# Kernel optimization log

Measured on AMD Instinct MI355X. Metric: run time of the kernel, lower is better.

The kernel has to match this reference:

```python
import jax, jax.numpy as jnp
import numpy as np

B, S, D, H = 4, 2048, 1024, 16
DK = D // H


def setup_inputs() -> dict:
    key = jax.random.key(0)
    ks = jax.random.split(key, 5)
    scale = 1.0 / np.sqrt(D)
    return {
        "x": jax.random.normal(ks[0], (B, S, D), dtype=jnp.float32),
        "w_q": jax.random.normal(ks[1], (D, D), dtype=jnp.float32) * scale,
        "w_k": jax.random.normal(ks[2], (D, D), dtype=jnp.float32) * scale,
        "w_v": jax.random.normal(ks[3], (D, D), dtype=jnp.float32) * scale,
        "w_o": jax.random.normal(ks[4], (D, D), dtype=jnp.float32) * scale,
        "b_o": jnp.zeros((D,), dtype=jnp.float32),
    }


def reference(x, w_q, w_k, w_v, w_o, b_o):
    b, s, d = x.shape
    # Projections (torch Linear: x @ W.T); split into heads -> [b, h, s, dk]
    q = (x @ w_q.T).reshape(b, s, H, DK).transpose(0, 2, 1, 3)
    k = (x @ w_k.T).reshape(b, s, H, DK).transpose(0, 2, 1, 3)
    v = (x @ w_v.T).reshape(b, s, H, DK).transpose(0, 2, 1, 3)
    # Scores [b, h, s, s]; causal mask (strict upper triangle -> -inf), then scale.
    scores = jnp.einsum("bhqd,bhkd->bhqk", q, k)
    causal = jnp.triu(jnp.ones((s, s), dtype=bool), k=1)
    scores = jnp.where(causal, -jnp.inf, scores)
    attn = jax.nn.softmax(scores / np.sqrt(DK), axis=-1)
    out = jnp.einsum("bhqk,bhkd->bhqd", attn, v)
    out = out.transpose(0, 2, 1, 3).reshape(b, s, d)
    return out @ w_o.T + b_o
```

## Files before the change

kernel.cpp:

```cpp
#include <hip/hip_runtime.h>
#include <hip/hip_bf16.h>
#include <math.h>

#define GLOBAL_AS __attribute__((address_space(1)))
#define LDS_AS __attribute__((address_space(3)))

typedef __bf16 bf16x8 __attribute__((ext_vector_type(8)));
typedef __bf16 bf16x4 __attribute__((ext_vector_type(4)));
typedef float f32x4 __attribute__((ext_vector_type(4)));
typedef float f32x16 __attribute__((ext_vector_type(16)));
typedef unsigned short u16x8 __attribute__((ext_vector_type(8)));

static constexpr int BB = 4, SS = 2048, DD = 1024, HH = 16, DKK = 64;
static constexpr int MM = BB * SS;
static constexpr int NQKV = 3 * DD;
static constexpr int NQT = SS / 128;

__device__ inline unsigned int cvt_pk_bf16(float lo, float hi) {
  unsigned int r;
  asm("v_cvt_pk_bf16_f32 %0, %1, %2" : "=v"(r) : "v"(lo), "v"(hi));
  return r;
}

__global__ __launch_bounds__(256) void cvt_kernel(const float* __restrict__ in,
                                                  __bf16* __restrict__ out,
                                                  int n4) {
  int i = blockIdx.x * blockDim.x + threadIdx.x;
  if (i < n4) {
    float4 v = reinterpret_cast<const float4*>(in)[i];
    bf16x4 o;
    o[0] = (__bf16)v.x; o[1] = (__bf16)v.y; o[2] = (__bf16)v.z; o[3] = (__bf16)v.w;
    *reinterpret_cast<bf16x4*>(out + (size_t)i * 4) = o;
  }
}

__global__ __launch_bounds__(256) void cvtw_kernel(const float* __restrict__ w_q,
                                                   const float* __restrict__ w_k,
                                                   const float* __restrict__ w_v,
                                                   const float* __restrict__ w_o,
                                                   __bf16* __restrict__ w_qkv,
                                                   __bf16* __restrict__ w_obf) {
  const int sel = blockIdx.y;
  const float* src = (sel == 0) ? w_q : (sel == 1) ? w_k : (sel == 2) ? w_v : w_o;
  __bf16* dst = (sel < 3) ? (w_qkv + (size_t)sel * DD * DD) : w_obf;
  int i = blockIdx.x * blockDim.x + threadIdx.x;
  float4 v = reinterpret_cast<const float4*>(src)[i];
  bf16x4 o;
  o[0] = (__bf16)v.x; o[1] = (__bf16)v.y; o[2] = (__bf16)v.z; o[3] = (__bf16)v.w;
  *reinterpret_cast<bf16x4*>(dst + (size_t)i * 4) = o;
}

template <int MODE>
__global__ __launch_bounds__(512, 1) void gemm8p(const unsigned short* __restrict__ A,
                                                 const unsigned short* __restrict__ Bm,
                                                 void* __restrict__ Cout,
                                                 const float* __restrict__ bias,
                                                 unsigned short* __restrict__ vt,
                                                 int Ndim, int K) {
  __shared__ __align__(16) unsigned short Asm[2 * 2 * 4096];
  __shared__ __align__(16) unsigned short Bsm[2 * 2 * 8192];
  const int tid = threadIdx.x, wid = tid >> 6, ln = tid & 63;
  const int wm = wid >> 2, wn = wid & 3;
  const int cl = ln & 15, ck = ln >> 4;

  const int gx = gridDim.x;
  const int nwg = gx * gridDim.y;
  const int qch = nwg >> 3;
  int lid = blockIdx.y * gx + blockIdx.x;
  lid = (lid & 7) * qch + (lid >> 3);
  const int bn0 = (lid % gx) * 256;
  const int bm0 = (lid / gx) * 128;

  const int KT = K >> 6;
  const int sr = tid >> 2;
  const int scol = ((tid & 3) ^ (sr & 3)) << 3;
  const int sc8 = (ck ^ (cl & 3)) << 3;

  f32x4 acc[4][4] = {};

  auto stage_group = [&](int buf, int kt, int kk) {
    const int k0 = kt * 64 + kk * 32;
    const unsigned short* ga = A + (size_t)(bm0 + sr) * K + k0 + scol;
    __builtin_amdgcn_global_load_lds((GLOBAL_AS void*)ga,
        (LDS_AS void*)(Asm + (buf * 2 + kk) * 4096 + wid * 512), 16, 0, 0);
#pragma unroll
    for (int j = 0; j < 2; ++j) {
      const unsigned short* gb = Bm + (size_t)(bn0 + j * 128 + sr) * K + k0 + scol;
      __builtin_amdgcn_global_load_lds((GLOBAL_AS void*)gb,
          (LDS_AS void*)(Bsm + (buf * 2 + kk) * 8192 + j * 4096 + wid * 512), 16, 0, 0);
    }
  };

  auto phase = [&](int p, int kk, int g_buf, int g_kt, int g_kk, bool g_issue, int vm) {
    bf16x8 af[4], bfr[4];
    const unsigned short* ab = Asm + (p * 2 + kk) * 4096;
    const unsigned short* bb = Bsm + (p * 2 + kk) * 8192;
#pragma unroll
    for (int mf = 0; mf < 4; ++mf)
      af[mf] = *reinterpret_cast<const bf16x8*>(ab + (wm * 64 + mf * 16 + cl) * 32 + sc8);
#pragma unroll
    for (int nf = 0; nf < 4; ++nf)
      bfr[nf] = *reinterpret_cast<const bf16x8*>(bb + (wn * 64 + nf * 16 + cl) * 32 + sc8);
    if (g_issue) stage_group(g_buf, g_kt, g_kk);
    __builtin_amdgcn_s_barrier();
    __builtin_amdgcn_s_setprio(1);
#pragma unroll
    for (int mf = 0; mf < 4; ++mf)
#pragma unroll
      for (int nf = 0; nf < 4; ++nf)
        acc[mf][nf] = __builtin_amdgcn_mfma_f32_16x16x32_bf16(af[mf], bfr[nf], acc[mf][nf], 0, 0, 0);
    __builtin_amdgcn_s_setprio(0);
    if (vm == 6)      asm volatile("s_waitcnt vmcnt(6)" ::: "memory");
    else if (vm == 3) asm volatile("s_waitcnt vmcnt(3)" ::: "memory");
    else if (vm == 0) asm volatile("s_waitcnt vmcnt(0)" ::: "memory");
    __builtin_amdgcn_s_barrier();
  };

  stage_group(0, 0, 0);
  stage_group(0, 0, 1);
  stage_group(1, 1, 0);
  asm volatile("s_waitcnt vmcnt(6)" ::: "memory");
  __builtin_amdgcn_s_barrier();

  for (int kt = 0; kt < KT; ++kt) {
    const int p = kt & 1;
    const bool i0 = (kt + 1 < KT);
    const bool i1 = (kt + 2 < KT);
    phase(p, 0, p ^ 1, kt + 1, 1, i0, i0 ? 6 : 0);
    phase(p, 1, p, kt + 2, 0, i1, (kt < KT - 1) ? (i1 ? 6 : 3) : -1);
  }

#pragma unroll
  for (int mf = 0; mf < 4; ++mf) {
#pragma unroll
    for (int nf = 0; nf < 4; ++nf) {
      const int col = bn0 + wn * 64 + nf * 16 + cl;
      if constexpr (MODE == 2) {
        if (col >= 2 * DD) {
          const int hcol = col - 2 * DD;
          const int hh = hcol >> 6, dk = hcol & 63;
          const int row0 = bm0 + wm * 64 + mf * 16 + ck * 4;
          const int bb_ = row0 >> 11, s0 = row0 & 2047;
          bf16x4 pv;
#pragma unroll
          for (int r = 0; r < 4; ++r) pv[r] = (__bf16)acc[mf][nf][r];
          *reinterpret_cast<bf16x4*>(vt + ((size_t)((bb_ * HH + hh) * 64 + dk)) * SS + s0) = pv;
          continue;
        }
      }
#pragma unroll
      for (int r = 0; r < 4; ++r) {
        const int row = bm0 + wm * 64 + mf * 16 + ck * 4 + r;
        float v = acc[mf][nf][r];
        if constexpr (MODE == 0) {
          ((float*)Cout)[(size_t)row * Ndim + col] = v + bias[col];
        } else {
          if (col < DD) v *= 0.18033688011112042f;
          ((__bf16*)Cout)[(size_t)row * Ndim + col] = (__bf16)v;
        }
      }
    }
  }
}

__global__ __launch_bounds__(256) void attn_kernel(const unsigned short* __restrict__ qkv,
                                                   const unsigned short* __restrict__ vt,
                                                   unsigned short* __restrict__ attn_out) {
  const int pi = blockIdx.x, h = blockIdx.y, b = blockIdx.z;
  const int tid = threadIdx.x, wv = tid >> 6, ln = tid & 63;
  const int l31 = ln & 31, hi = ln >> 5;
  const int bh = b * HH + h;

  __shared__ __align__(16) unsigned short Ks[2][64 * 64];
  __shared__ __align__(16) unsigned short Vs[2][64 * 64];

  bf16x8 vones;
#pragma unroll
  for (int j = 0; j < 8; ++j) vones[j] = (__bf16)1.0f;

  auto stage = [&](int bsel, int kv0s) {
#pragma unroll
    for (int i = 0; i < 2; ++i) {
      int idx = wv * 2 + i;
      int row = idx * 8 + (ln >> 3);
      int sch = (ln & 7) ^ (row & 7);
      const unsigned short* gk = qkv + ((size_t)(b * SS + kv0s + row) * NQKV + DD + h * DKK + sch * 8);
      __builtin_amdgcn_global_load_lds((GLOBAL_AS void*)gk, (LDS_AS void*)(&Ks[bsel][idx * 512]), 16, 0, 0);
      const unsigned short* gv = vt + ((size_t)(bh * 64 + row) * SS + kv0s + sch * 8);
      __builtin_amdgcn_global_load_lds((GLOBAL_AS void*)gv, (LDS_AS void*)(&Vs[bsel][idx * 512]), 16, 0, 0);
    }
  };

  auto process = [&](int qt) {
    const int q0w = qt * 128 + wv * 32;
    const int qq = q0w + l31;

    bf16x8 qf[4];
#pragma unroll
    for (int kkk = 0; kkk < 4; ++kkk)
      qf[kkk] = *reinterpret_cast<const bf16x8*>(
          qkv + (size_t)(b * SS + qq) * NQKV + h * DKK + kkk * 16 + hi * 8);

    f32x16 ot[2] = {};
    f32x16 lsum = {};
    float mrow = -INFINITY;

    const int nt = 2 * qt + 2;
    stage(0, 0);
    __syncthreads();
    int buf = 0;

    for (int t = 0; t < nt; ++t) {
      const int kv0 = t * 64;
      if (t + 1 < nt) stage(buf ^ 1, (t + 1) * 64);

      if (kv0 <= q0w + 31) {
        const unsigned short* kb = &Ks[buf][0];
        const unsigned short* vb = &Vs[buf][0];

        f32x16 st[2];
        __builtin_amdgcn_s_setprio(1);
#pragma unroll
        for (int cc = 0; cc < 2; ++cc) {
          f32x16 z = {};
#pragma unroll
          for (int kkk = 0; kkk < 4; ++kkk) {
            bf16x8 kf = *reinterpret_cast<const bf16x8*>(
                kb + (cc * 32 + l31) * 64 + (((kkk * 2 + hi) ^ (l31 & 7)) * 8));
            z = __builtin_amdgcn_mfma_f32_32x32x16_bf16(kf, qf[kkk], z, 0, 0, 0);
          }
          st[cc] = z;
        }
        __builtin_amdgcn_s_setprio(0);

        if (kv0 + 63 > q0w) {
          const int kvb = kv0 + 4 * hi;
#pragma unroll
          for (int cc = 0; cc < 2; ++cc)
#pragma unroll
            for (int r = 0; r < 16; ++r) {
              const int kv = kvb + cc * 32 + (r & 3) + 8 * (r >> 2);
              st[cc][r] = (kv <= qq) ? st[cc][r] : -INFINITY;
            }
        }

        float tm = st[0][0];
#pragma unroll
        for (int r = 1; r < 16; ++r) tm = fmaxf(tm, st[0][r]);
#pragma unroll
        for (int r = 0; r < 16; ++r) tm = fmaxf(tm, st[1][r]);
        tm = fmaxf(tm, __shfl_xor(tm, 32));

        if (__any(tm - mrow > 8.0f)) {
          float mn = fmaxf(mrow, tm);
          float al = __builtin_amdgcn_exp2f(mrow - mn);
          mrow = mn;
          lsum *= al;
          ot[0] *= al;
          ot[1] *= al;
        }

#pragma unroll
        for (int cc = 0; cc < 2; ++cc)
#pragma unroll
          for (int r = 0; r < 16; ++r)
            st[cc][r] = __builtin_amdgcn_exp2f(st[cc][r] - mrow);

        unsigned int pk[2][4], pk2[2][4];
#pragma unroll
        for (int cc = 0; cc < 2; ++cc)
#pragma unroll
          for (int g = 0; g < 4; ++g) {
            pk[cc][g]  = cvt_pk_bf16(st[cc][4 * g + 0], st[cc][4 * g + 1]);
            pk2[cc][g] = cvt_pk_bf16(st[cc][4 * g + 2], st[cc][4 * g + 3]);
          }

        __builtin_amdgcn_s_setprio(1);
#pragma unroll
        for (int ks = 0; ks < 4; ++ks) {
          const int cc = ks >> 1, g0 = 2 * (ks & 1), g1 = g0 + 1;
          unsigned int Aw = pk[cc][g0], Bw = pk[cc][g1];
          asm volatile("v_permlane32_swap_b32 %0, %1" : "+v"(Aw), "+v"(Bw));
          unsigned int A2 = pk2[cc][g0], B2 = pk2[cc][g1];
          asm volatile("v_permlane32_swap_b32 %0, %1" : "+v"(A2), "+v"(B2));
          union { unsigned int u[4]; bf16x8 v; } pb;
          pb.u[0] = Aw; pb.u[1] = A2; pb.u[2] = Bw; pb.u[3] = B2;
          lsum = __builtin_amdgcn_mfma_f32_32x32x16_bf16(vones, pb.v, lsum, 0, 0, 0);
#pragma unroll
          for (int dc = 0; dc < 2; ++dc) {
            bf16x8 vf = *reinterpret_cast<const bf16x8*>(
                vb + (dc * 32 + l31) * 64 + (((ks * 2 + hi) ^ (l31 & 7)) * 8));
            ot[dc] = __builtin_amdgcn_mfma_f32_32x32x16_bf16(vf, pb.v, ot[dc], 0, 0, 0);
          }
        }
        __builtin_amdgcn_s_setprio(0);
      }

      __syncthreads();
      buf ^= 1;
    }

    const float inv = 1.0f / lsum[0];
    __bf16* aout = (__bf16*)attn_out + (size_t)(b * SS + qq) * DD + h * DKK;
#pragma unroll
    for (int dc = 0; dc < 2; ++dc)
#pragma unroll
      for (int g = 0; g < 4; ++g) {
        uint2 pw;
        pw.x = cvt_pk_bf16(ot[dc][4 * g + 0] * inv, ot[dc][4 * g + 1] * inv);
        pw.y = cvt_pk_bf16(ot[dc][4 * g + 2] * inv, ot[dc][4 * g + 3] * inv);
        *reinterpret_cast<uint2*>(aout + dc * 32 + 4 * hi + 8 * g) = pw;
      }
  };

  process(NQT - 1 - pi);
  process(pi);
}

extern "C" void kernel_launch(void* const* d_in, const int* in_sizes, int n_in,
                              void* d_out, int out_size, void* d_ws, size_t ws_size,
                              hipStream_t stream) {
  const float* x = (const float*)d_in[0];
  const float* w_q = (const float*)d_in[1];
  const float* w_k = (const float*)d_in[2];
  const float* w_v = (const float*)d_in[3];
  const float* w_o = (const float*)d_in[4];
  const float* b_o = (const float*)d_in[5];
  float* out = (float*)d_out;

  unsigned short* ws = (unsigned short*)d_ws;
  unsigned short* x_bf = ws;
  unsigned short* w_qkv = x_bf + (size_t)MM * DD;
  unsigned short* w_obf = w_qkv + (size_t)NQKV * DD;
  unsigned short* qkv = w_obf + (size_t)DD * DD;
  unsigned short* vt = qkv + (size_t)MM * NQKV;
  unsigned short* attn = vt + (size_t)BB * HH * DKK * SS;

  cvt_kernel<<<(MM * DD / 4 + 255) / 256, 256, 0, stream>>>(x, (__bf16*)x_bf, MM * DD / 4);
  cvtw_kernel<<<dim3(DD * DD / 4 / 256, 4), 256, 0, stream>>>(w_q, w_k, w_v, w_o,
                                                              (__bf16*)w_qkv, (__bf16*)w_obf);

  gemm8p<2><<<dim3(NQKV / 256, MM / 128), 512, 0, stream>>>(x_bf, w_qkv, qkv, nullptr, vt, NQKV, DD);

  attn_kernel<<<dim3(NQT / 2, HH, BB), 256, 0, stream>>>(qkv, vt, attn);

  gemm8p<0><<<dim3(DD / 256, MM / 128), 512, 0, stream>>>(attn, w_obf, out, b_o, nullptr, DD, DD);
}
```

Measured before the change: 188.9 us.

## Use 256x256 tiled GEMM with interleaved LDS pipeline for QKV projection

Replaces the 128x256-tile QKV projection GEMM with a dedicated 256x256-tile kernel. It uses an 8-phase schedule that interleaves global-to-LDS loads of the next K-step with MFMA work on the current one, and raises wave priority around the MFMA blocks. The larger tile doubles operand reuse per byte loaded and halves the workgroup count to 384. The cost is more registers and LDS per block, fewer workgroups for the 256 CUs (tail imbalance), and many barriers. The output GEMM is de-templated and keeps the old kernel.

```diff
diff --git a/kernel.cpp b/kernel.cpp
--- a/kernel.cpp
+++ b/kernel.cpp
@@ -50,12 +50,161 @@
   *reinterpret_cast<bf16x4*>(dst + (size_t)i * 4) = o;
 }
 
-template <int MODE>
+__global__ __launch_bounds__(512, 1) void gemm256(const unsigned short* __restrict__ A,
+                                                  const unsigned short* __restrict__ Bm,
+                                                  unsigned short* __restrict__ qkv,
+                                                  unsigned short* __restrict__ vt,
+                                                  int Ndim, int K) {
+  __shared__ __align__(16) unsigned short SA[2][2][8192];
+  __shared__ __align__(16) unsigned short SB[2][2][8192];
+  const int tid = threadIdx.x, wid = tid >> 6, ln = tid & 63;
+  const int wm = wid >> 2, wn = wid & 3;
+  const int cl = ln & 15, ck = ln >> 4;
+
+  const int gx = gridDim.x, nwg = gx * gridDim.y;
+  const int qch = nwg >> 3;
+  int lid = blockIdx.y * gx + blockIdx.x;
+  lid = (lid & 7) * qch + (lid >> 3);
+  const int bn0 = (lid % gx) * 256;
+  const int bm0 = (lid / gx) * 256;
+
+  const int KT = K >> 6;
+  const int srow = tid >> 3;
+  const int scol8 = (((tid & 7) ^ (srow & 7)) << 3);
+  int chk[2];
+  chk[0] = ((ck ^ (cl & 7)) << 3);
+  chk[1] = (((4 + ck) ^ (cl & 7)) << 3);
+
+  f32x4 acc[8][4] = {};
+  bf16x8 aR[4][2], bRa[2][2], bRb[2][2];
+
+  auto stA = [&](int t, int qa) {
+    const unsigned short* g = A + (size_t)(bm0 + qa * 64 + srow) * K + t * 64 + scol8;
+    __builtin_amdgcn_global_load_lds((GLOBAL_AS void*)g,
+        (LDS_AS void*)(&SA[t & 1][qa >> 1][(qa & 1) * 4096 + tid * 8]), 16, 0, 0);
+  };
+  auto stB = [&](int t, int qb) {
+    const unsigned short* g = Bm + (size_t)(bn0 + qb * 64 + srow) * K + t * 64 + scol8;
+    __builtin_amdgcn_global_load_lds((GLOBAL_AS void*)g,
+        (LDS_AS void*)(&SB[t & 1][qb >> 1][(qb & 1) * 4096 + tid * 8]), 16, 0, 0);
+  };
+  auto ldA = [&](int buf, int rh) {
+    const unsigned short* base = &SA[buf][wm][0];
+#pragma unroll
+    for (int rf = 0; rf < 4; ++rf) {
+      const int row = rh * 64 + rf * 16 + cl;
+#pragma unroll
+      for (int kk = 0; kk < 2; ++kk)
+        aR[rf][kk] = *reinterpret_cast<const bf16x8*>(base + row * 64 + chk[kk]);
+    }
+  };
+  auto ldB = [&](int buf, int chalf, bf16x8 (&br)[2][2]) {
+    const unsigned short* base = &SB[buf][wn >> 1][0];
+#pragma unroll
+    for (int cf = 0; cf < 2; ++cf) {
+      const int row = (wn & 1) * 64 + chalf * 32 + cf * 16 + cl;
+#pragma unroll
+      for (int kk = 0; kk < 2; ++kk)
+        br[cf][kk] = *reinterpret_cast<const bf16x8*>(base + row * 64 + chk[kk]);
+    }
+  };
+  auto MF = [&](int rh, int chalf, bf16x8 (&br)[2][2]) {
+    __builtin_amdgcn_s_setprio(1);
+#pragma unroll
+    for (int rf = 0; rf < 4; ++rf)
+#pragma unroll
+      for (int cf = 0; cf < 2; ++cf)
+#pragma unroll
+        for (int kk = 0; kk < 2; ++kk)
+          acc[rh * 4 + rf][chalf * 2 + cf] = __builtin_amdgcn_mfma_f32_16x16x32_bf16(
+              aR[rf][kk], br[cf][kk], acc[rh * 4 + rf][chalf * 2 + cf], 0, 0, 0);
+    __builtin_amdgcn_s_setprio(0);
+  };
+
+  stB(0, 0); stB(0, 1); stB(0, 2); stB(0, 3);
+  stA(0, 0); stA(0, 2); stA(0, 1); stA(0, 3);
+  asm volatile("s_waitcnt vmcnt(2)" ::: "memory");
+  __builtin_amdgcn_s_barrier();
+
+  const int HKT = KT >> 1;
+  for (int it = 0; it < HKT; ++it) {
+    const int t1 = 2 * it + 1, v = 2 * it + 2;
+    const bool hv = (v < KT);
+    ldA(0, 0); ldB(0, 0, bRa);
+    stB(t1, 0); stB(t1, 1);
+    __builtin_amdgcn_s_barrier();
+    MF(0, 0, bRa);
+    __builtin_amdgcn_s_barrier();
+    ldB(0, 1, bRb);
+    stB(t1, 2); stB(t1, 3);
+    __builtin_amdgcn_s_barrier();
+    MF(0, 1, bRb);
+    asm volatile("s_waitcnt vmcnt(4)" ::: "memory");
+    __builtin_amdgcn_s_barrier();
+    ldA(0, 1);
+    stA(t1, 0); stA(t1, 2);
+    __builtin_amdgcn_s_barrier();
+    MF(1, 1, bRb);
+    __builtin_amdgcn_s_barrier();
+    stA(t1, 1); stA(t1, 3);
+    __builtin_amdgcn_s_barrier();
+    MF(1, 0, bRa);
+    asm volatile("s_waitcnt vmcnt(2)" ::: "memory");
+    __builtin_amdgcn_s_barrier();
+    ldA(1, 0); ldB(1, 0, bRa);
+    if (hv) { stB(v, 0); stB(v, 1); }
+    __builtin_amdgcn_s_barrier();
+    MF(0, 0, bRa);
+    __builtin_amdgcn_s_barrier();
+    ldB(1, 1, bRb);
+    if (hv) { stB(v, 2); stB(v, 3); }
+    __builtin_amdgcn_s_barrier();
+    MF(0, 1, bRb);
+    if (hv) asm volatile("s_waitcnt vmcnt(4)" ::: "memory");
+    else    asm volatile("s_waitcnt vmcnt(0)" ::: "memory");
+    __builtin_amdgcn_s_barrier();
+    ldA(1, 1);
+    if (hv) { stA(v, 0); stA(v, 2); }
+    __builtin_amdgcn_s_barrier();
+    MF(1, 1, bRb);
+    __builtin_amdgcn_s_barrier();
+    if (hv) { stA(v, 1); stA(v, 3); }
+    __builtin_amdgcn_s_barrier();
+    MF(1, 0, bRa);
+    if (hv) asm volatile("s_waitcnt vmcnt(2)" ::: "memory");
+    __builtin_amdgcn_s_barrier();
+  }
+
+#pragma unroll
+  for (int rf8 = 0; rf8 < 8; ++rf8) {
+#pragma unroll
+    for (int cf4 = 0; cf4 < 4; ++cf4) {
+      const int col = bn0 + wn * 64 + cf4 * 16 + cl;
+      const int row0 = bm0 + wm * 128 + rf8 * 16 + ck * 4;
+      if (col >= 2 * DD) {
+        const int hcol = col - 2 * DD;
+        const int hh = hcol >> 6, dk = hcol & 63;
+        const int bb_ = row0 >> 11, s0 = row0 & 2047;
+        bf16x4 pv;
+#pragma unroll
+        for (int r = 0; r < 4; ++r) pv[r] = (__bf16)acc[rf8][cf4][r];
+        *reinterpret_cast<bf16x4*>(vt + ((size_t)((bb_ * HH + hh) * 64 + dk)) * SS + s0) = pv;
+      } else {
+#pragma unroll
+        for (int r = 0; r < 4; ++r) {
+          float vv = acc[rf8][cf4][r];
+          if (col < DD) vv *= 0.18033688011112042f;
+          ((__bf16*)qkv)[(size_t)(row0 + r) * Ndim + col] = (__bf16)vv;
+        }
+      }
+    }
+  }
+}
+
 __global__ __launch_bounds__(512, 1) void gemm8p(const unsigned short* __restrict__ A,
                                                  const unsigned short* __restrict__ Bm,
-                                                 void* __restrict__ Cout,
+                                                 float* __restrict__ Cout,
                                                  const float* __restrict__ bias,
-                                                 unsigned short* __restrict__ vt,
                                                  int Ndim, int K) {
   __shared__ __align__(16) unsigned short Asm[2 * 2 * 4096];
   __shared__ __align__(16) unsigned short Bsm[2 * 2 * 8192];
@@ -135,29 +284,10 @@
 #pragma unroll
     for (int nf = 0; nf < 4; ++nf) {
       const int col = bn0 + wn * 64 + nf * 16 + cl;
-      if constexpr (MODE == 2) {
-        if (col >= 2 * DD) {
-          const int hcol = col - 2 * DD;
-          const int hh = hcol >> 6, dk = hcol & 63;
-          const int row0 = bm0 + wm * 64 + mf * 16 + ck * 4;
-          const int bb_ = row0 >> 11, s0 = row0 & 2047;
-          bf16x4 pv;
-#pragma unroll
-          for (int r = 0; r < 4; ++r) pv[r] = (__bf16)acc[mf][nf][r];
-          *reinterpret_cast<bf16x4*>(vt + ((size_t)((bb_ * HH + hh) * 64 + dk)) * SS + s0) = pv;
-          continue;
-        }
-      }
 #pragma unroll
       for (int r = 0; r < 4; ++r) {
         const int row = bm0 + wm * 64 + mf * 16 + ck * 4 + r;
-        float v = acc[mf][nf][r];
-        if constexpr (MODE == 0) {
-          ((float*)Cout)[(size_t)row * Ndim + col] = v + bias[col];
-        } else {
-          if (col < DD) v *= 0.18033688011112042f;
-          ((__bf16*)Cout)[(size_t)row * Ndim + col] = (__bf16)v;
-        }
+        Cout[(size_t)row * Ndim + col] = acc[mf][nf][r] + bias[col];
       }
     }
   }
@@ -340,9 +470,9 @@
   cvtw_kernel<<<dim3(DD * DD / 4 / 256, 4), 256, 0, stream>>>(w_q, w_k, w_v, w_o,
                                                               (__bf16*)w_qkv, (__bf16*)w_obf);
 
-  gemm8p<2><<<dim3(NQKV / 256, MM / 128), 512, 0, stream>>>(x_bf, w_qkv, qkv, nullptr, vt, NQKV, DD);
+  gemm256<<<dim3(NQKV / 256, MM / 256), 512, 0, stream>>>(x_bf, w_qkv, qkv, vt, NQKV, DD);
 
   attn_kernel<<<dim3(NQT / 2, HH, BB), 256, 0, stream>>>(qkv, vt, attn);
 
-  gemm8p<0><<<dim3(DD / 256, MM / 128), 512, 0, stream>>>(attn, w_obf, out, b_o, nullptr, DD, DD);
-}
+  gemm8p<<<dim3(DD / 256, MM / 128), 512, 0, stream>>>(attn, w_obf, out, b_o, DD, DD);
+}
```

Result: no change. 190.6 us (+0.9%).

## Replace pipelined 128x256 GEMM with simpler 128x128 multi-block-per-CU GEMM

Applied to the files above, without the earlier changes.

Swaps the hand-pipelined double-buffered 512-thread 128x256 GEMM for a 256-thread 128x128 tile kernel. The new kernel stages the full 64-wide K slice at once, uses an 8-way XOR swizzle, and has no software prefetch. It syncs twice per K step and relies on three resident blocks per CU to hide latency instead of explicit overlap. The tiles are smaller, so there are more workgroups and more redundant loads of the operands.

```diff
diff --git a/kernel.cpp b/kernel.cpp
--- a/kernel.cpp
+++ b/kernel.cpp
@@ -51,83 +51,73 @@
 }
 
 template <int MODE>
-__global__ __launch_bounds__(512, 1) void gemm8p(const unsigned short* __restrict__ A,
-                                                 const unsigned short* __restrict__ Bm,
-                                                 void* __restrict__ Cout,
-                                                 const float* __restrict__ bias,
-                                                 unsigned short* __restrict__ vt,
-                                                 int Ndim, int K) {
-  __shared__ __align__(16) unsigned short Asm[2 * 2 * 4096];
-  __shared__ __align__(16) unsigned short Bsm[2 * 2 * 8192];
-  const int tid = threadIdx.x, wid = tid >> 6, ln = tid & 63;
-  const int wm = wid >> 2, wn = wid & 3;
+__global__ __launch_bounds__(256, 3) void gemm128(const unsigned short* __restrict__ A,
+                                                  const unsigned short* __restrict__ Bm,
+                                                  void* __restrict__ Cout,
+                                                  const float* __restrict__ bias,
+                                                  unsigned short* __restrict__ vt,
+                                                  int Ndim, int K) {
+  __shared__ __align__(16) unsigned short SA[128 * 64];
+  __shared__ __align__(16) unsigned short SB[128 * 64];
+  const int tid = threadIdx.x, wv = tid >> 6, ln = tid & 63;
+  const int wm = wv >> 1, wn = wv & 1;
   const int cl = ln & 15, ck = ln >> 4;
 
-  const int gx = gridDim.x;
-  const int nwg = gx * gridDim.y;
+  const int gx = gridDim.x, nwg = gx * gridDim.y;
   const int qch = nwg >> 3;
   int lid = blockIdx.y * gx + blockIdx.x;
   lid = (lid & 7) * qch + (lid >> 3);
-  const int bn0 = (lid % gx) * 256;
+  const int bn0 = (lid % gx) * 128;
   const int bm0 = (lid / gx) * 128;
 
   const int KT = K >> 6;
-  const int sr = tid >> 2;
-  const int scol = ((tid & 3) ^ (sr & 3)) << 3;
-  const int sc8 = (ck ^ (cl & 3)) << 3;
+  const int sr = tid >> 3;
+  int chk[2];
+  chk[0] = ((ck ^ (cl & 7)) << 3);
+  chk[1] = (((4 + ck) ^ (cl & 7)) << 3);
 
   f32x4 acc[4][4] = {};
 
-  auto stage_group = [&](int buf, int kt, int kk) {
-    const int k0 = kt * 64 + kk * 32;
-    const unsigned short* ga = A + (size_t)(bm0 + sr) * K + k0 + scol;
-    __builtin_amdgcn_global_load_lds((GLOBAL_AS void*)ga,
-        (LDS_AS void*)(Asm + (buf * 2 + kk) * 4096 + wid * 512), 16, 0, 0);
-#pragma unroll
-    for (int j = 0; j < 2; ++j) {
-      const unsigned short* gb = Bm + (size_t)(bn0 + j * 128 + sr) * K + k0 + scol;
+  for (int kt = 0; kt < KT; ++kt) {
+    const int k0 = kt * 64;
+#pragma unroll
+    for (int i = 0; i < 4; ++i) {
+      const int row = i * 32 + sr;
+      const int sc = (((tid & 7) ^ (row & 7)) << 3);
+      const unsigned short* ga = A + (size_t)(bm0 + row) * K + k0 + sc;
+      __builtin_amdgcn_global_load_lds((GLOBAL_AS void*)ga,
+          (LDS_AS void*)(SA + i * 2048 + tid * 8), 16, 0, 0);
+      const unsigned short* gb = Bm + (size_t)(bn0 + row) * K + k0 + sc;
       __builtin_amdgcn_global_load_lds((GLOBAL_AS void*)gb,
-          (LDS_AS void*)(Bsm + (buf * 2 + kk) * 8192 + j * 4096 + wid * 512), 16, 0, 0);
-    }
-  };
-
-  auto phase = [&](int p, int kk, int g_buf, int g_kt, int g_kk, bool g_issue, int vm) {
-    bf16x8 af[4], bfr[4];
-    const unsigned short* ab = Asm + (p * 2 + kk) * 4096;
-    const unsigned short* bb = Bsm + (p * 2 + kk) * 8192;
+          (LDS_AS void*)(SB + i * 2048 + tid * 8), 16, 0, 0);
+    }
+    __syncthreads();
+
+    bf16x8 af[4][2], bf[4][2];
+#pragma unroll
+    for (int mf = 0; mf < 4; ++mf) {
+      const int row = wm * 64 + mf * 16 + cl;
+#pragma unroll
+      for (int kk = 0; kk < 2; ++kk)
+        af[mf][kk] = *reinterpret_cast<const bf16x8*>(SA + row * 64 + chk[kk]);
+    }
+#pragma unroll
+    for (int nf = 0; nf < 4; ++nf) {
+      const int row = wn * 64 + nf * 16 + cl;
+#pragma unroll
+      for (int kk = 0; kk < 2; ++kk)
+        bf[nf][kk] = *reinterpret_cast<const bf16x8*>(SB + row * 64 + chk[kk]);
+    }
+    __builtin_amdgcn_s_setprio(1);
 #pragma unroll
     for (int mf = 0; mf < 4; ++mf)
-      af[mf] = *reinterpret_cast<const bf16x8*>(ab + (wm * 64 + mf * 16 + cl) * 32 + sc8);
-#pragma unroll
-    for (int nf = 0; nf < 4; ++nf)
-      bfr[nf] = *reinterpret_cast<const bf16x8*>(bb + (wn * 64 + nf * 16 + cl) * 32 + sc8);
-    if (g_issue) stage_group(g_buf, g_kt, g_kk);
-    __builtin_amdgcn_s_barrier();
-    __builtin_amdgcn_s_setprio(1);
-#pragma unroll
-    for (int mf = 0; mf < 4; ++mf)
 #pragma unroll
       for (int nf = 0; nf < 4; ++nf)
-        acc[mf][nf] = __builtin_amdgcn_mfma_f32_16x16x32_bf16(af[mf], bfr[nf], acc[mf][nf], 0, 0, 0);
+#pragma unroll
+        for (int kk = 0; kk < 2; ++kk)
+          acc[mf][nf] = __builtin_amdgcn_mfma_f32_16x16x32_bf16(af[mf][kk], bf[nf][kk], acc[mf][nf], 0, 0, 0);
     __builtin_amdgcn_s_setprio(0);
-    if (vm == 6)      asm volatile("s_waitcnt vmcnt(6)" ::: "memory");
-    else if (vm == 3) asm volatile("s_waitcnt vmcnt(3)" ::: "memory");
-    else if (vm == 0) asm volatile("s_waitcnt vmcnt(0)" ::: "memory");
-    __builtin_amdgcn_s_barrier();
-  };
-
-  stage_group(0, 0, 0);
-  stage_group(0, 0, 1);
-  stage_group(1, 1, 0);
-  asm volatile("s_waitcnt vmcnt(6)" ::: "memory");
-  __builtin_amdgcn_s_barrier();
-
-  for (int kt = 0; kt < KT; ++kt) {
-    const int p = kt & 1;
-    const bool i0 = (kt + 1 < KT);
-    const bool i1 = (kt + 2 < KT);
-    phase(p, 0, p ^ 1, kt + 1, 1, i0, i0 ? 6 : 0);
-    phase(p, 1, p, kt + 2, 0, i1, (kt < KT - 1) ? (i1 ? 6 : 3) : -1);
+    __syncthreads();
   }
 
 #pragma unroll
@@ -135,11 +125,11 @@
 #pragma unroll
     for (int nf = 0; nf < 4; ++nf) {
       const int col = bn0 + wn * 64 + nf * 16 + cl;
+      const int row0 = bm0 + wm * 64 + mf * 16 + ck * 4;
       if constexpr (MODE == 2) {
         if (col >= 2 * DD) {
           const int hcol = col - 2 * DD;
           const int hh = hcol >> 6, dk = hcol & 63;
-          const int row0 = bm0 + wm * 64 + mf * 16 + ck * 4;
           const int bb_ = row0 >> 11, s0 = row0 & 2047;
           bf16x4 pv;
 #pragma unroll
@@ -150,13 +140,12 @@
       }
 #pragma unroll
       for (int r = 0; r < 4; ++r) {
-        const int row = bm0 + wm * 64 + mf * 16 + ck * 4 + r;
         float v = acc[mf][nf][r];
         if constexpr (MODE == 0) {
-          ((float*)Cout)[(size_t)row * Ndim + col] = v + bias[col];
+          ((float*)Cout)[(size_t)(row0 + r) * Ndim + col] = v + bias[col];
         } else {
           if (col < DD) v *= 0.18033688011112042f;
-          ((__bf16*)Cout)[(size_t)row * Ndim + col] = (__bf16)v;
+          ((__bf16*)Cout)[(size_t)(row0 + r) * Ndim + col] = (__bf16)v;
         }
       }
     }
@@ -340,9 +329,9 @@
   cvtw_kernel<<<dim3(DD * DD / 4 / 256, 4), 256, 0, stream>>>(w_q, w_k, w_v, w_o,
                                                               (__bf16*)w_qkv, (__bf16*)w_obf);
 
-  gemm8p<2><<<dim3(NQKV / 256, MM / 128), 512, 0, stream>>>(x_bf, w_qkv, qkv, nullptr, vt, NQKV, DD);
+  gemm128<2><<<dim3(NQKV / 128, MM / 128), 256, 0, stream>>>(x_bf, w_qkv, qkv, nullptr, vt, NQKV, DD);
 
   attn_kernel<<<dim3(NQT / 2, HH, BB), 256, 0, stream>>>(qkv, vt, attn);
 
-  gemm8p<0><<<dim3(DD / 256, MM / 128), 512, 0, stream>>>(attn, w_obf, out, b_o, nullptr, DD, DD);
-}
+  gemm128<0><<<dim3(DD / 128, MM / 128), 256, 0, stream>>>(attn, w_obf, out, b_o, nullptr, DD, DD);
+}
```

New measurement: 166.8 us. 11.7% less time.
